# Kernel optimization log

Measured on AMD Instinct MI355X. Metric: run time of the kernel, lower is better.

Reference implementation:

```python
import jax, jax.numpy as jnp
import numpy as np

NUM_LAYERS = 8
HIDDEN = 1000
INPUT = 2


def _uniform(key, shape, bound):
    return jax.random.uniform(key, shape, jnp.float32, -bound, bound)


def setup_inputs() -> dict:
    key = jax.random.key(0)
    ks = jax.random.split(key, 12)
    bound = 1.0 / np.sqrt(HIDDEN)
    inp = {
        "input": jax.random.normal(ks[0], (INPUT,), jnp.float32),
        "hiddens": jax.random.normal(ks[1], (NUM_LAYERS, 1, HIDDEN), jnp.float32),
        # GRU params, PyTorch gate order (r, z, n)
        "W_ih0": _uniform(ks[2], (3 * HIDDEN, INPUT), bound),            # layer 0 input weights
        "W_ih": _uniform(ks[3], (NUM_LAYERS - 1, 3 * HIDDEN, HIDDEN), bound),  # layers 1..7
        "W_hh": _uniform(ks[4], (NUM_LAYERS, 3 * HIDDEN, HIDDEN), bound),
        "b_ih": _uniform(ks[5], (NUM_LAYERS, 3 * HIDDEN), bound),
        "b_hh": _uniform(ks[6], (NUM_LAYERS, 3 * HIDDEN), bound),
        # output head 1000 -> 1
        "W_out": _uniform(ks[7], (1, HIDDEN), bound),
        "b_out": _uniform(ks[8], (1,), bound),
    }
    return inp


def _gru_cell(x, h, Wih, Whh, bih, bhh):
    gi = Wih @ x + bih                      # (3H,)
    gh = Whh @ h + bhh                      # (3H,)
    ir, iz, i_n = jnp.split(gi, 3)
    hr, hz, h_n = jnp.split(gh, 3)
    r = jax.nn.sigmoid(ir + hr)
    z = jax.nn.sigmoid(iz + hz)
    n = jnp.tanh(i_n + r * h_n)
    return (1.0 - z) * n + z * h


def reference(input, hiddens, W_ih0, W_ih, W_hh, b_ih, b_hh, W_out, b_out):
    x = input.reshape(-1)                   # (2,) single timestep, batch=1
    h_prev = hiddens[:, 0, :]               # (L, H)
    new_h = []
    layer_in = x
    for l in range(NUM_LAYERS):
        Wih_l = W_ih0 if l == 0 else W_ih[l - 1]
        h_l = _gru_cell(layer_in, h_prev[l], Wih_l, W_hh[l], b_ih[l], b_hh[l])
        new_h.append(h_l)
        layer_in = h_l                      # no dropout (inference semantics)
    flow = (W_out @ layer_in + b_out).reshape(1, 1, 1)
    hiddens_prime = jnp.stack(new_h)[:, None, :]   # (L, 1, H)
    return flow, hiddens_prime
```

## Files before the change

kernel.cpp:

```cpp
#include <hip/hip_runtime.h>
#include <math.h>

#define HIDDEN 1000
#define K4 250

__device__ __forceinline__ float sigmoidf_(float x) {
  return 1.f / (1.f + expf(-x));
}

__device__ __forceinline__ float wave_dot1000(const float* __restrict__ w,
                                              const float* __restrict__ v,
                                              int lane) {
  const float4* w4 = reinterpret_cast<const float4*>(w);
  const float4* v4 = reinterpret_cast<const float4*>(v);
  float acc = 0.f;
  for (int c = lane; c < K4; c += 64) {
    float4 a = w4[c];
    float4 b = v4[c];
    acc = fmaf(a.x, b.x, acc);
    acc = fmaf(a.y, b.y, acc);
    acc = fmaf(a.z, b.z, acc);
    acc = fmaf(a.w, b.w, acc);
  }
  #pragma unroll
  for (int off = 32; off; off >>= 1) acc += __shfl_xor(acc, off);
  return acc;
}

__global__ void gru_phaseA(const float* __restrict__ x,
                           const float* __restrict__ hiddens,
                           const float* __restrict__ Wih0,
                           const float* __restrict__ Whh,
                           const float* __restrict__ bih,
                           const float* __restrict__ bhh,
                           float* __restrict__ gh_ws,
                           float* __restrict__ h_buf,
                           float* __restrict__ out)
{
  const int wave = threadIdx.x >> 6;
  const int lane = threadIdx.x & 63;
  const int b = blockIdx.x;

  if (b < 250) {
    const int j = b * 4 + wave;
    const float* h0 = hiddens;
    float ghr = wave_dot1000(Whh + (size_t)(j)        * HIDDEN, h0, lane) + bhh[j];
    float ghz = wave_dot1000(Whh + (size_t)(1000 + j) * HIDDEN, h0, lane) + bhh[1000 + j];
    float ghn = wave_dot1000(Whh + (size_t)(2000 + j) * HIDDEN, h0, lane) + bhh[2000 + j];
    if (lane == 0) {
      const float x0 = x[0], x1 = x[1];
      float gir = Wih0[2*j]        * x0 + Wih0[2*j+1]        * x1 + bih[j];
      float giz = Wih0[2*(1000+j)] * x0 + Wih0[2*(1000+j)+1] * x1 + bih[1000 + j];
      float gin = Wih0[2*(2000+j)] * x0 + Wih0[2*(2000+j)+1] * x1 + bih[2000 + j];
      float r = sigmoidf_(gir + ghr);
      float z = sigmoidf_(giz + ghz);
      float n = tanhf(gin + r * ghn);
      float h = (1.f - z) * n + z * h0[j];
      h_buf[j] = h;
      out[1 + j] = h;
    }
  } else {
    const int rg = (b - 250) * 4 + wave;
    const int l = rg / 3000 + 1;
    const int r = rg % 3000;
    const float* hl = hiddens + (size_t)l * HIDDEN;
    float gh = wave_dot1000(Whh + ((size_t)l * 3000 + r) * HIDDEN, hl, lane)
             + bhh[l * 3000 + r];
    if (lane == 0) gh_ws[rg] = gh;
  }
}

__global__ __launch_bounds__(256)
void gru_layer2(const int l,
                const float* __restrict__ hiddens,
                const float* __restrict__ Wih,
                const float* __restrict__ bih,
                const float* __restrict__ gh_ws,
                float* __restrict__ h_buf,
                float* __restrict__ out)
{
  const int t = threadIdx.x;
  const int j = blockIdx.x;
  const float4* W4  = reinterpret_cast<const float4*>(
      Wih + (size_t)(l - 1) * 3000 * HIDDEN);
  const float4* hin = reinterpret_cast<const float4*>(
      h_buf + (size_t)(l - 1) * HIDDEN);

  float aR = 0.f, aZ = 0.f, aN = 0.f;
  if (t < K4) {
    float4 hv = hin[t];
    float4 wr = W4[(size_t)(j)        * K4 + t];
    float4 wz = W4[(size_t)(1000 + j) * K4 + t];
    float4 wn = W4[(size_t)(2000 + j) * K4 + t];
    aR = fmaf(wr.x, hv.x, fmaf(wr.y, hv.y, fmaf(wr.z, hv.z, wr.w * hv.w)));
    aZ = fmaf(wz.x, hv.x, fmaf(wz.y, hv.y, fmaf(wz.z, hv.z, wz.w * hv.w)));
    aN = fmaf(wn.x, hv.x, fmaf(wn.y, hv.y, fmaf(wn.z, hv.z, wn.w * hv.w)));
  }
  #pragma unroll
  for (int off = 32; off; off >>= 1) {
    aR += __shfl_xor(aR, off);
    aZ += __shfl_xor(aZ, off);
    aN += __shfl_xor(aN, off);
  }
  __shared__ float s[4][3];
  const int wave = t >> 6, lane = t & 63;
  if (lane == 0) { s[wave][0] = aR; s[wave][1] = aZ; s[wave][2] = aN; }
  __syncthreads();
  if (t == 0) {
    float gir = s[0][0] + s[1][0] + s[2][0] + s[3][0] + bih[l*3000 + j];
    float giz = s[0][1] + s[1][1] + s[2][1] + s[3][1] + bih[l*3000 + 1000 + j];
    float gin = s[0][2] + s[1][2] + s[2][2] + s[3][2] + bih[l*3000 + 2000 + j];
    float ghr = gh_ws[(l-1)*3000 + j];
    float ghz = gh_ws[(l-1)*3000 + 1000 + j];
    float ghn = gh_ws[(l-1)*3000 + 2000 + j];
    float r = sigmoidf_(gir + ghr);
    float z = sigmoidf_(giz + ghz);
    float n = tanhf(gin + r * ghn);
    float h = (1.f - z) * n + z * hiddens[(size_t)l * HIDDEN + j];
    h_buf[l * HIDDEN + j] = h;
    out[1 + l * HIDDEN + j] = h;
  }
}

__global__ void gru_flow(const float* __restrict__ Wout,
                         const float* __restrict__ bout,
                         const float* __restrict__ h_buf,
                         float* __restrict__ out)
{
  const int t = threadIdx.x;
  const float* h7 = h_buf + 7 * HIDDEN;
  float acc = 0.f;
  for (int i = t; i < HIDDEN; i += 256) acc += Wout[i] * h7[i];
  #pragma unroll
  for (int off = 32; off; off >>= 1) acc += __shfl_xor(acc, off);
  __shared__ float s[4];
  const int wave = t >> 6, lane = t & 63;
  if (lane == 0) s[wave] = acc;
  __syncthreads();
  if (t == 0) out[0] = s[0] + s[1] + s[2] + s[3] + bout[0];
}

extern "C" void kernel_launch(void* const* d_in, const int* in_sizes, int n_in,
                              void* d_out, int out_size, void* d_ws, size_t ws_size,
                              hipStream_t stream) {
  const float* x       = (const float*)d_in[0];
  const float* hiddens = (const float*)d_in[1];
  const float* Wih0    = (const float*)d_in[2];
  const float* Wih     = (const float*)d_in[3];
  const float* Whh     = (const float*)d_in[4];
  const float* bih     = (const float*)d_in[5];
  const float* bhh     = (const float*)d_in[6];
  const float* Wout    = (const float*)d_in[7];
  const float* bout    = (const float*)d_in[8];
  float* out   = (float*)d_out;
  float* gh_ws = (float*)d_ws;
  float* h_buf = gh_ws + 21000;

  gru_phaseA<<<5500, 256, 0, stream>>>(x, hiddens, Wih0, Whh, bih, bhh,
                                       gh_ws, h_buf, out);
  for (int l = 1; l < 8; ++l) {
    gru_layer2<<<1000, 256, 0, stream>>>(l, hiddens, Wih, bih, gh_ws, h_buf, out);
  }
  gru_flow<<<1, 256, 0, stream>>>(Wout, bout, h_buf, out);
}
```

Measured before the change: 59.05 us.

## Remap phase A to one block per hidden unit and fuse output head via atomics

```diff
diff --git a/kernel.cpp b/kernel.cpp
--- a/kernel.cpp
+++ b/kernel.cpp
@@ -8,65 +8,84 @@
   return 1.f / (1.f + expf(-x));
 }
 
-__device__ __forceinline__ float wave_dot1000(const float* __restrict__ w,
-                                              const float* __restrict__ v,
-                                              int lane) {
-  const float4* w4 = reinterpret_cast<const float4*>(w);
-  const float4* v4 = reinterpret_cast<const float4*>(v);
-  float acc = 0.f;
-  for (int c = lane; c < K4; c += 64) {
-    float4 a = w4[c];
-    float4 b = v4[c];
-    acc = fmaf(a.x, b.x, acc);
-    acc = fmaf(a.y, b.y, acc);
-    acc = fmaf(a.z, b.z, acc);
-    acc = fmaf(a.w, b.w, acc);
+__device__ __forceinline__ void block_dot3(const float4* __restrict__ row0,
+                                           const float4* __restrict__ row1,
+                                           const float4* __restrict__ row2,
+                                           const float4* __restrict__ hv4,
+                                           int t, float& r0, float& r1, float& r2) {
+  float a0 = 0.f, a1 = 0.f, a2 = 0.f;
+  if (t < K4) {
+    float4 hv = hv4[t];
+    float4 w0 = row0[t];
+    float4 w1 = row1[t];
+    float4 w2 = row2[t];
+    a0 = fmaf(w0.x, hv.x, fmaf(w0.y, hv.y, fmaf(w0.z, hv.z, w0.w * hv.w)));
+    a1 = fmaf(w1.x, hv.x, fmaf(w1.y, hv.y, fmaf(w1.z, hv.z, w1.w * hv.w)));
+    a2 = fmaf(w2.x, hv.x, fmaf(w2.y, hv.y, fmaf(w2.z, hv.z, w2.w * hv.w)));
   }
   #pragma unroll
-  for (int off = 32; off; off >>= 1) acc += __shfl_xor(acc, off);
-  return acc;
+  for (int off = 32; off; off >>= 1) {
+    a0 += __shfl_xor(a0, off);
+    a1 += __shfl_xor(a1, off);
+    a2 += __shfl_xor(a2, off);
+  }
+  __shared__ float s[4][3];
+  const int wave = t >> 6, lane = t & 63;
+  if (lane == 0) { s[wave][0] = a0; s[wave][1] = a1; s[wave][2] = a2; }
+  __syncthreads();
+  if (t == 0) {
+    r0 = s[0][0] + s[1][0] + s[2][0] + s[3][0];
+    r1 = s[0][1] + s[1][1] + s[2][1] + s[3][1];
+    r2 = s[0][2] + s[1][2] + s[2][2] + s[3][2];
+  }
 }
 
-__global__ void gru_phaseA(const float* __restrict__ x,
-                           const float* __restrict__ hiddens,
-                           const float* __restrict__ Wih0,
-                           const float* __restrict__ Whh,
-                           const float* __restrict__ bih,
-                           const float* __restrict__ bhh,
-                           float* __restrict__ gh_ws,
-                           float* __restrict__ h_buf,
-                           float* __restrict__ out)
+__global__ __launch_bounds__(256)
+void gru_phaseA(const float* __restrict__ x,
+                const float* __restrict__ hiddens,
+                const float* __restrict__ Wih0,
+                const float* __restrict__ Whh,
+                const float* __restrict__ bih,
+                const float* __restrict__ bhh,
+                const float* __restrict__ bout,
+                float* __restrict__ gh_ws,
+                float* __restrict__ h_buf,
+                float* __restrict__ out)
 {
-  const int wave = threadIdx.x >> 6;
-  const int lane = threadIdx.x & 63;
+  const int t = threadIdx.x;
   const int b = blockIdx.x;
+  const int l = b / 1000;
+  const int j = b - l * 1000;
 
-  if (b < 250) {
-    const int j = b * 4 + wave;
-    const float* h0 = hiddens;
-    float ghr = wave_dot1000(Whh + (size_t)(j)        * HIDDEN, h0, lane) + bhh[j];
-    float ghz = wave_dot1000(Whh + (size_t)(1000 + j) * HIDDEN, h0, lane) + bhh[1000 + j];
-    float ghn = wave_dot1000(Whh + (size_t)(2000 + j) * HIDDEN, h0, lane) + bhh[2000 + j];
-    if (lane == 0) {
+  const float4* W4 = reinterpret_cast<const float4*>(
+      Whh + (size_t)l * 3000 * HIDDEN);
+  const float4* hv4 = reinterpret_cast<const float4*>(
+      hiddens + (size_t)l * HIDDEN);
+
+  float ghr, ghz, ghn;
+  block_dot3(W4 + (size_t)(j)        * K4,
+             W4 + (size_t)(1000 + j) * K4,
+             W4 + (size_t)(2000 + j) * K4,
+             hv4, t, ghr, ghz, ghn);
+
+  if (t == 0) {
+    if (l == 0) {
       const float x0 = x[0], x1 = x[1];
       float gir = Wih0[2*j]        * x0 + Wih0[2*j+1]        * x1 + bih[j];
       float giz = Wih0[2*(1000+j)] * x0 + Wih0[2*(1000+j)+1] * x1 + bih[1000 + j];
       float gin = Wih0[2*(2000+j)] * x0 + Wih0[2*(2000+j)+1] * x1 + bih[2000 + j];
-      float r = sigmoidf_(gir + ghr);
-      float z = sigmoidf_(giz + ghz);
-      float n = tanhf(gin + r * ghn);
-      float h = (1.f - z) * n + z * h0[j];
+      float r = sigmoidf_(gir + ghr + bhh[j]);
+      float z = sigmoidf_(giz + ghz + bhh[1000 + j]);
+      float n = tanhf(gin + r * (ghn + bhh[2000 + j]));
+      float h = (1.f - z) * n + z * hiddens[j];
       h_buf[j] = h;
       out[1 + j] = h;
+      if (j == 0) out[0] = bout[0];
+    } else {
+      gh_ws[(l-1)*3000 + j]        = ghr + bhh[l*3000 + j];
+      gh_ws[(l-1)*3000 + 1000 + j] = ghz + bhh[l*3000 + 1000 + j];
+      gh_ws[(l-1)*3000 + 2000 + j] = ghn + bhh[l*3000 + 2000 + j];
     }
-  } else {
-    const int rg = (b - 250) * 4 + wave;
-    const int l = rg / 3000 + 1;
-    const int r = rg % 3000;
-    const float* hl = hiddens + (size_t)l * HIDDEN;
-    float gh = wave_dot1000(Whh + ((size_t)l * 3000 + r) * HIDDEN, hl, lane)
-             + bhh[l * 3000 + r];
-    if (lane == 0) gh_ws[rg] = gh;
   }
 }
 
@@ -76,6 +95,7 @@
                 const float* __restrict__ Wih,
                 const float* __restrict__ bih,
                 const float* __restrict__ gh_ws,
+                const float* __restrict__ Wout,
                 float* __restrict__ h_buf,
                 float* __restrict__ out)
 {
@@ -86,58 +106,24 @@
   const float4* hin = reinterpret_cast<const float4*>(
       h_buf + (size_t)(l - 1) * HIDDEN);
 
-  float aR = 0.f, aZ = 0.f, aN = 0.f;
-  if (t < K4) {
-    float4 hv = hin[t];
-    float4 wr = W4[(size_t)(j)        * K4 + t];
-    float4 wz = W4[(size_t)(1000 + j) * K4 + t];
-    float4 wn = W4[(size_t)(2000 + j) * K4 + t];
-    aR = fmaf(wr.x, hv.x, fmaf(wr.y, hv.y, fmaf(wr.z, hv.z, wr.w * hv.w)));
-    aZ = fmaf(wz.x, hv.x, fmaf(wz.y, hv.y, fmaf(wz.z, hv.z, wz.w * hv.w)));
-    aN = fmaf(wn.x, hv.x, fmaf(wn.y, hv.y, fmaf(wn.z, hv.z, wn.w * hv.w)));
-  }
-  #pragma unroll
-  for (int off = 32; off; off >>= 1) {
-    aR += __shfl_xor(aR, off);
-    aZ += __shfl_xor(aZ, off);
-    aN += __shfl_xor(aN, off);
-  }
-  __shared__ float s[4][3];
-  const int wave = t >> 6, lane = t & 63;
-  if (lane == 0) { s[wave][0] = aR; s[wave][1] = aZ; s[wave][2] = aN; }
-  __syncthreads();
+  float gir, giz, gin;
+  block_dot3(W4 + (size_t)(j)        * K4,
+             W4 + (size_t)(1000 + j) * K4,
+             W4 + (size_t)(2000 + j) * K4,
+             hin, t, gir, giz, gin);
+
   if (t == 0) {
-    float gir = s[0][0] + s[1][0] + s[2][0] + s[3][0] + bih[l*3000 + j];
-    float giz = s[0][1] + s[1][1] + s[2][1] + s[3][1] + bih[l*3000 + 1000 + j];
-    float gin = s[0][2] + s[1][2] + s[2][2] + s[3][2] + bih[l*3000 + 2000 + j];
     float ghr = gh_ws[(l-1)*3000 + j];
     float ghz = gh_ws[(l-1)*3000 + 1000 + j];
     float ghn = gh_ws[(l-1)*3000 + 2000 + j];
-    float r = sigmoidf_(gir + ghr);
-    float z = sigmoidf_(giz + ghz);
-    float n = tanhf(gin + r * ghn);
+    float r = sigmoidf_(gir + bih[l*3000 + j] + ghr);
+    float z = sigmoidf_(giz + bih[l*3000 + 1000 + j] + ghz);
+    float n = tanhf(gin + bih[l*3000 + 2000 + j] + r * ghn);
     float h = (1.f - z) * n + z * hiddens[(size_t)l * HIDDEN + j];
     h_buf[l * HIDDEN + j] = h;
     out[1 + l * HIDDEN + j] = h;
+    if (l == 7) atomicAdd(&out[0], Wout[j] * h);
   }
-}
-
-__global__ void gru_flow(const float* __restrict__ Wout,
-                         const float* __restrict__ bout,
-                         const float* __restrict__ h_buf,
-                         float* __restrict__ out)
-{
-  const int t = threadIdx.x;
-  const float* h7 = h_buf + 7 * HIDDEN;
-  float acc = 0.f;
-  for (int i = t; i < HIDDEN; i += 256) acc += Wout[i] * h7[i];
-  #pragma unroll
-  for (int off = 32; off; off >>= 1) acc += __shfl_xor(acc, off);
-  __shared__ float s[4];
-  const int wave = t >> 6, lane = t & 63;
-  if (lane == 0) s[wave] = acc;
-  __syncthreads();
-  if (t == 0) out[0] = s[0] + s[1] + s[2] + s[3] + bout[0];
 }
 
 extern "C" void kernel_launch(void* const* d_in, const int* in_sizes, int n_in,
@@ -156,10 +142,10 @@
   float* gh_ws = (float*)d_ws;
   float* h_buf = gh_ws + 21000;
 
-  gru_phaseA<<<5500, 256, 0, stream>>>(x, hiddens, Wih0, Whh, bih, bhh,
+  gru_phaseA<<<8000, 256, 0, stream>>>(x, hiddens, Wih0, Whh, bih, bhh, bout,
                                        gh_ws, h_buf, out);
   for (int l = 1; l < 8; ++l) {
-    gru_layer2<<<1000, 256, 0, stream>>>(l, hiddens, Wih, bih, gh_ws, h_buf, out);
+    gru_layer2<<<1000, 256, 0, stream>>>(l, hiddens, Wih, bih, gh_ws, Wout,
+                                         h_buf, out);
   }
-  gru_flow<<<1, 256, 0, stream>>>(Wout, bout, h_buf, out);
 }
```

New measurement: 66.81 us. 13.1% more time.

## Prefetch W_ih into cache during phase A and fuse output head via atomics

Applied to the files above, without the earlier changes.

```diff
diff --git a/kernel.cpp b/kernel.cpp
--- a/kernel.cpp
+++ b/kernel.cpp
@@ -3,6 +3,7 @@
 
 #define HIDDEN 1000
 #define K4 250
+#define WARMB 2048
 
 __device__ __forceinline__ float sigmoidf_(float x) {
   return 1.f / (1.f + expf(-x));
@@ -30,9 +31,11 @@
 __global__ void gru_phaseA(const float* __restrict__ x,
                            const float* __restrict__ hiddens,
                            const float* __restrict__ Wih0,
+                           const float* __restrict__ Wih,
                            const float* __restrict__ Whh,
                            const float* __restrict__ bih,
                            const float* __restrict__ bhh,
+                           const float* __restrict__ bout,
                            float* __restrict__ gh_ws,
                            float* __restrict__ h_buf,
                            float* __restrict__ out)
@@ -58,8 +61,9 @@
       float h = (1.f - z) * n + z * h0[j];
       h_buf[j] = h;
       out[1 + j] = h;
+      if (j == 0) out[0] = bout[0];
     }
-  } else {
+  } else if (b < 5500) {
     const int rg = (b - 250) * 4 + wave;
     const int l = rg / 3000 + 1;
     const int r = rg % 3000;
@@ -67,6 +71,16 @@
     float gh = wave_dot1000(Whh + ((size_t)l * 3000 + r) * HIDDEN, hl, lane)
              + bhh[l * 3000 + r];
     if (lane == 0) gh_ws[rg] = gh;
+  } else {
+    const float4* WI4 = reinterpret_cast<const float4*>(Wih);
+    const size_t NW4 = (size_t)7 * 3000 * K4;
+    size_t idx = (size_t)(b - 5500) * 256 + threadIdx.x;
+    float acc = 0.f;
+    for (; idx < NW4; idx += (size_t)WARMB * 256) {
+      float4 w = WI4[idx];
+      acc += w.x + w.y + w.z + w.w;
+    }
+    asm volatile("" :: "v"(acc));
   }
 }
 
@@ -76,6 +90,7 @@
                 const float* __restrict__ Wih,
                 const float* __restrict__ bih,
                 const float* __restrict__ gh_ws,
+                const float* __restrict__ Wout,
                 float* __restrict__ h_buf,
                 float* __restrict__ out)
 {
@@ -119,25 +134,8 @@
     float h = (1.f - z) * n + z * hiddens[(size_t)l * HIDDEN + j];
     h_buf[l * HIDDEN + j] = h;
     out[1 + l * HIDDEN + j] = h;
+    if (l == 7) atomicAdd(&out[0], Wout[j] * h);
   }
-}
-
-__global__ void gru_flow(const float* __restrict__ Wout,
-                         const float* __restrict__ bout,
-                         const float* __restrict__ h_buf,
-                         float* __restrict__ out)
-{
-  const int t = threadIdx.x;
-  const float* h7 = h_buf + 7 * HIDDEN;
-  float acc = 0.f;
-  for (int i = t; i < HIDDEN; i += 256) acc += Wout[i] * h7[i];
-  #pragma unroll
-  for (int off = 32; off; off >>= 1) acc += __shfl_xor(acc, off);
-  __shared__ float s[4];
-  const int wave = t >> 6, lane = t & 63;
-  if (lane == 0) s[wave] = acc;
-  __syncthreads();
-  if (t == 0) out[0] = s[0] + s[1] + s[2] + s[3] + bout[0];
 }
 
 extern "C" void kernel_launch(void* const* d_in, const int* in_sizes, int n_in,
@@ -156,10 +154,10 @@
   float* gh_ws = (float*)d_ws;
   float* h_buf = gh_ws + 21000;
 
-  gru_phaseA<<<5500, 256, 0, stream>>>(x, hiddens, Wih0, Whh, bih, bhh,
-                                       gh_ws, h_buf, out);
+  gru_phaseA<<<5500 + WARMB, 256, 0, stream>>>(x, hiddens, Wih0, Wih, Whh,
+                                               bih, bhh, bout, gh_ws, h_buf, out);
   for (int l = 1; l < 8; ++l) {
-    gru_layer2<<<1000, 256, 0, stream>>>(l, hiddens, Wih, bih, gh_ws, h_buf, out);
+    gru_layer2<<<1000, 256, 0, stream>>>(l, hiddens, Wih, bih, gh_ws, Wout,
+                                         h_buf, out);
   }
-  gru_flow<<<1, 256, 0, stream>>>(Wout, bout, h_buf, out);
 }
```

Measured after the change: 78.81 us. +33.5%, slower.
